# Performance work log

Hardware: AMD Instinct MI355X
Metric: run time of the kernel (lower is better)

The kernel has to match this reference:

```python
import jax, jax.numpy as jnp
import numpy as np

# Neighbor offsets (di, dj) implied by each 3x3 kernel: out_j = gray - shift(gray, di, dj)
# kernel0..kernel7 as defined in the torch module (center weight +1, one neighbor -1)
OFFSETS = [(0, -1), (1, -1), (1, 0), (1, 1), (0, 1), (-1, 1), (-1, 0), (-1, -1)]
EPS = 1e-5  # torch InstanceNorm2d default


def setup_inputs() -> dict:
    key = jax.random.key(0)
    x = jax.random.uniform(key, (8, 3, 1024, 1024), dtype=jnp.float32)
    return {"x": x}


def _ltpe(x):
    # RGB -> gray, [B,1,H,W]
    g = (0.3 * x[:, 0] + 0.59 * x[:, 1] + 0.11 * x[:, 2])[:, None]
    B, _, H, W = g.shape
    gp = jnp.pad(g, ((0, 0), (0, 0), (1, 1), (1, 1)))  # zero pad = conv padding=1
    out = jnp.zeros_like(g)
    for j, (di, dj) in enumerate(OFFSETS):
        nb = gp[:, :, 1 + di:1 + di + H, 1 + dj:1 + dj + W]
        d = (g - nb + 1.0) * 0.5          # (conv_out + 1) * 0.5
        out = out + d * (float(2 ** j) / 255.0)
    # InstanceNorm2d(1): per (b, c) mean/biased-var over spatial dims, no affine
    mean = jnp.mean(out, axis=(2, 3), keepdims=True)
    var = jnp.var(out, axis=(2, 3), keepdims=True)
    out = (out - mean) * jax.lax.rsqrt(var + EPS)
    return jnp.concatenate([out, out, out], axis=1)  # [B,3,H,W]


def reference(x):
    return _ltpe(x)
```

## Files before the change

kernel.cpp:

```cpp
#include <hip/hip_runtime.h>
#include <math.h>

constexpr int H = 1024, W = 1024, B = 8;
constexpr int NPIX = H * W;

__device__ __forceinline__ float grayat(const float* __restrict__ xb, int r, int c) {
    const float* p = xb + (size_t)r * W + c;
    return 0.3f * p[0] + 0.59f * p[NPIX] + 0.11f * p[2 * NPIX];
}

__global__ __launch_bounds__(256)
void ltpe_stage1(const float* __restrict__ x, float* __restrict__ out,
                 float2* __restrict__ part)
{
    const int b    = blockIdx.y;
    const int k    = blockIdx.x;
    const int r    = ((k & 7) << 7) | (k >> 3);
    const int tid  = threadIdx.x;
    const int c    = tid << 2;
    const int lane = tid & 63;

    const float* xb = x + (size_t)b * 3 * NPIX;

    float4 g[3];
    #pragma unroll
    for (int dr = 0; dr < 3; ++dr) {
        const int rr = r + dr - 1;
        float4 q0 = {0.f,0.f,0.f,0.f}, q1 = q0, q2 = q0;
        if ((unsigned)rr < (unsigned)H) {
            const float* p = xb + (size_t)rr * W + c;
            q0 = *reinterpret_cast<const float4*>(p);
            q1 = *reinterpret_cast<const float4*>(p + NPIX);
            q2 = *reinterpret_cast<const float4*>(p + 2 * NPIX);
        }
        g[dr].x = 0.3f * q0.x + 0.59f * q1.x + 0.11f * q2.x;
        g[dr].y = 0.3f * q0.y + 0.59f * q1.y + 0.11f * q2.y;
        g[dr].z = 0.3f * q0.z + 0.59f * q1.z + 0.11f * q2.z;
        g[dr].w = 0.3f * q0.w + 0.59f * q1.w + 0.11f * q2.w;
    }

    float gl[3], gr[3];
    #pragma unroll
    for (int dr = 0; dr < 3; ++dr) {
        gl[dr] = __shfl_up(g[dr].w, 1);
        gr[dr] = __shfl_down(g[dr].x, 1);
    }
    if (lane == 0) {
        #pragma unroll
        for (int dr = 0; dr < 3; ++dr) {
            const int rr = r + dr - 1;
            gl[dr] = (c > 0 && (unsigned)rr < (unsigned)H) ? grayat(xb, rr, c - 1) : 0.f;
        }
    }
    if (lane == 63) {
        #pragma unroll
        for (int dr = 0; dr < 3; ++dr) {
            const int rr = r + dr - 1;
            gr[dr] = (c + 4 < W && (unsigned)rr < (unsigned)H) ? grayat(xb, rr, c + 4) : 0.f;
        }
    }

    float up[6], mi[6], dn[6];
    up[0]=gl[0]; up[1]=g[0].x; up[2]=g[0].y; up[3]=g[0].z; up[4]=g[0].w; up[5]=gr[0];
    mi[0]=gl[1]; mi[1]=g[1].x; mi[2]=g[1].y; mi[3]=g[1].z; mi[4]=g[1].w; mi[5]=gr[1];
    dn[0]=gl[2]; dn[1]=g[2].x; dn[2]=g[2].y; dn[3]=g[2].z; dn[4]=g[2].w; dn[5]=gr[2];

    constexpr float w0 = 1.f/255.f,  w1 = 2.f/255.f,  w2 = 4.f/255.f,  w3 = 8.f/255.f,
                    w4 = 16.f/255.f, w5 = 32.f/255.f, w6 = 64.f/255.f, w7 = 128.f/255.f;
    float tv[4];
    #pragma unroll
    for (int kk = 0; kk < 4; ++kk) {
        float s = w0 * mi[kk];
        s = fmaf(w1, dn[kk],     s);
        s = fmaf(w2, dn[kk + 1], s);
        s = fmaf(w3, dn[kk + 2], s);
        s = fmaf(w4, mi[kk + 2], s);
        s = fmaf(w5, up[kk + 2], s);
        s = fmaf(w6, up[kk + 1], s);
        s = fmaf(w7, up[kk],     s);
        tv[kk] = 0.5f * mi[kk + 1] + 0.5f - 0.5f * s;
    }

    float4 t4 = {tv[0], tv[1], tv[2], tv[3]};
    *reinterpret_cast<float4*>(out + (size_t)b * 3 * NPIX + (size_t)r * W + c) = t4;

    float s  = tv[0] + tv[1] + tv[2] + tv[3];
    float ss = tv[0]*tv[0] + tv[1]*tv[1] + tv[2]*tv[2] + tv[3]*tv[3];
    #pragma unroll
    for (int off = 32; off >= 1; off >>= 1) {
        s  += __shfl_down(s, off);
        ss += __shfl_down(ss, off);
    }
    __shared__ float2 wred[4];
    if (lane == 0) wred[tid >> 6] = make_float2(s, ss);
    __syncthreads();
    if (tid == 0) {
        float2 a0 = wred[0], a1 = wred[1], a2 = wred[2], a3 = wred[3];
        part[(size_t)b * H + k] = make_float2(a0.x + a1.x + a2.x + a3.x,
                                              a0.y + a1.y + a2.y + a3.y);
    }
}

__global__ __launch_bounds__(256)
void ltpe_stage2(const float2* __restrict__ part, float* __restrict__ scal)
{
    const int b = blockIdx.x;
    const int tid = threadIdx.x;
    double s = 0.0, ss = 0.0;
    #pragma unroll
    for (int i = 0; i < 4; ++i) {
        float2 p = part[(size_t)b * H + tid + i * 256];
        s += (double)p.x; ss += (double)p.y;
    }
    #pragma unroll
    for (int off = 32; off >= 1; off >>= 1) {
        s  += __shfl_down(s, off);
        ss += __shfl_down(ss, off);
    }
    __shared__ double red[8];
    const int lane = tid & 63, wv = tid >> 6;
    if (lane == 0) { red[wv] = s; red[4 + wv] = ss; }
    __syncthreads();
    if (tid == 0) {
        const double S  = red[0] + red[1] + red[2] + red[3];
        const double SS = red[4] + red[5] + red[6] + red[7];
        const double n    = (double)NPIX;
        const double mean = S / n;
        const double var  = SS / n - mean * mean;
        scal[2 * b]     = (float)mean;
        scal[2 * b + 1] = (float)(1.0 / sqrt(var + 1e-5));
    }
}

__global__ __launch_bounds__(256)
void ltpe_stage3(float* __restrict__ out, const float* __restrict__ scal)
{
    const int b = blockIdx.y;
    const float mean = scal[2 * b];
    const float rstd = scal[2 * b + 1];
    const size_t base = (size_t)b * 3 * NPIX +
                        ((size_t)blockIdx.x * 256 + threadIdx.x) * 4;
    const float4 t4 = *reinterpret_cast<const float4*>(out + base);
    float4 y;
    y.x = (t4.x - mean) * rstd;
    y.y = (t4.y - mean) * rstd;
    y.z = (t4.z - mean) * rstd;
    y.w = (t4.w - mean) * rstd;
    *reinterpret_cast<float4*>(out + base)            = y;
    *reinterpret_cast<float4*>(out + base + NPIX)     = y;
    *reinterpret_cast<float4*>(out + base + 2 * NPIX) = y;
}

extern "C" void kernel_launch(void* const* d_in, const int* in_sizes, int n_in,
                              void* d_out, int out_size, void* d_ws, size_t ws_size,
                              hipStream_t stream)
{
    const float* x = (const float*)d_in[0];
    float* out = (float*)d_out;
    float2* part = (float2*)d_ws;
    float* scal  = (float*)((char*)d_ws + 65536);

    ltpe_stage1<<<dim3(H, B), 256, 0, stream>>>(x, out, part);
    ltpe_stage2<<<B, 256, 0, stream>>>(part, scal);
    ltpe_stage3<<<dim3(NPIX / 1024, B), 256, 0, stream>>>(out, scal);
}
```

Measured before the change: 55.93 us.

## Compute four rows per block in stage1 to reuse halo rows

Each stage1 block now handles four consecutive output rows and loads six input rows instead of three per row. This cuts redundant halo reads from 3x to 1.5x of the input and reduces the number of partial sums and blocks. The launch-bound occupancy hint is raised, and the stage2 reduction shrinks to one partial per thread. The trade-offs are higher register pressure from holding 18 float4 loads in flight and fewer total blocks (2048).

```diff
diff --git a/kernel.cpp b/kernel.cpp
--- a/kernel.cpp
+++ b/kernel.cpp
@@ -3,89 +3,99 @@
 
 constexpr int H = 1024, W = 1024, B = 8;
 constexpr int NPIX = H * W;
+constexpr int ROWS = 4;
+constexpr int RG   = H / ROWS;
 
 __device__ __forceinline__ float grayat(const float* __restrict__ xb, int r, int c) {
     const float* p = xb + (size_t)r * W + c;
     return 0.3f * p[0] + 0.59f * p[NPIX] + 0.11f * p[2 * NPIX];
 }
 
-__global__ __launch_bounds__(256)
+__global__ __launch_bounds__(256, 2)
 void ltpe_stage1(const float* __restrict__ x, float* __restrict__ out,
                  float2* __restrict__ part)
 {
     const int b    = blockIdx.y;
-    const int k    = blockIdx.x;
-    const int r    = ((k & 7) << 7) | (k >> 3);
+    const int r0   = blockIdx.x * ROWS;
     const int tid  = threadIdx.x;
     const int c    = tid << 2;
     const int lane = tid & 63;
-
     const float* xb = x + (size_t)b * 3 * NPIX;
 
-    float4 g[3];
+    float4 q[6][3];
     #pragma unroll
-    for (int dr = 0; dr < 3; ++dr) {
-        const int rr = r + dr - 1;
-        float4 q0 = {0.f,0.f,0.f,0.f}, q1 = q0, q2 = q0;
+    for (int i = 0; i < 6; ++i) {
+        const int rr = r0 - 1 + i;
+        float4 z = {0.f, 0.f, 0.f, 0.f};
+        q[i][0] = z; q[i][1] = z; q[i][2] = z;
         if ((unsigned)rr < (unsigned)H) {
             const float* p = xb + (size_t)rr * W + c;
-            q0 = *reinterpret_cast<const float4*>(p);
-            q1 = *reinterpret_cast<const float4*>(p + NPIX);
-            q2 = *reinterpret_cast<const float4*>(p + 2 * NPIX);
-        }
-        g[dr].x = 0.3f * q0.x + 0.59f * q1.x + 0.11f * q2.x;
-        g[dr].y = 0.3f * q0.y + 0.59f * q1.y + 0.11f * q2.y;
-        g[dr].z = 0.3f * q0.z + 0.59f * q1.z + 0.11f * q2.z;
-        g[dr].w = 0.3f * q0.w + 0.59f * q1.w + 0.11f * q2.w;
-    }
-
-    float gl[3], gr[3];
-    #pragma unroll
-    for (int dr = 0; dr < 3; ++dr) {
-        gl[dr] = __shfl_up(g[dr].w, 1);
-        gr[dr] = __shfl_down(g[dr].x, 1);
-    }
-    if (lane == 0) {
-        #pragma unroll
-        for (int dr = 0; dr < 3; ++dr) {
-            const int rr = r + dr - 1;
-            gl[dr] = (c > 0 && (unsigned)rr < (unsigned)H) ? grayat(xb, rr, c - 1) : 0.f;
+            q[i][0] = *reinterpret_cast<const float4*>(p);
+            q[i][1] = *reinterpret_cast<const float4*>(p + NPIX);
+            q[i][2] = *reinterpret_cast<const float4*>(p + 2 * NPIX);
         }
     }
-    if (lane == 63) {
+    float pl[6], pr[6];
+    #pragma unroll
+    for (int i = 0; i < 6; ++i) { pl[i] = 0.f; pr[i] = 0.f; }
+    if (lane == 0 && c > 0) {
         #pragma unroll
-        for (int dr = 0; dr < 3; ++dr) {
-            const int rr = r + dr - 1;
-            gr[dr] = (c + 4 < W && (unsigned)rr < (unsigned)H) ? grayat(xb, rr, c + 4) : 0.f;
+        for (int i = 0; i < 6; ++i) {
+            const int rr = r0 - 1 + i;
+            if ((unsigned)rr < (unsigned)H) pl[i] = grayat(xb, rr, c - 1);
+        }
+    }
+    if (lane == 63 && c + 4 < W) {
+        #pragma unroll
+        for (int i = 0; i < 6; ++i) {
+            const int rr = r0 - 1 + i;
+            if ((unsigned)rr < (unsigned)H) pr[i] = grayat(xb, rr, c + 4);
         }
     }
 
-    float up[6], mi[6], dn[6];
-    up[0]=gl[0]; up[1]=g[0].x; up[2]=g[0].y; up[3]=g[0].z; up[4]=g[0].w; up[5]=gr[0];
-    mi[0]=gl[1]; mi[1]=g[1].x; mi[2]=g[1].y; mi[3]=g[1].z; mi[4]=g[1].w; mi[5]=gr[1];
-    dn[0]=gl[2]; dn[1]=g[2].x; dn[2]=g[2].y; dn[3]=g[2].z; dn[4]=g[2].w; dn[5]=gr[2];
+    float g[6][6];
+    #pragma unroll
+    for (int i = 0; i < 6; ++i) {
+        const float4 a = q[i][0], d = q[i][1], e = q[i][2];
+        g[i][1] = 0.3f * a.x + 0.59f * d.x + 0.11f * e.x;
+        g[i][2] = 0.3f * a.y + 0.59f * d.y + 0.11f * e.y;
+        g[i][3] = 0.3f * a.z + 0.59f * d.z + 0.11f * e.z;
+        g[i][4] = 0.3f * a.w + 0.59f * d.w + 0.11f * e.w;
+        float l  = __shfl_up(g[i][4], 1);
+        float rt = __shfl_down(g[i][1], 1);
+        if (lane == 0)  l  = pl[i];
+        if (lane == 63) rt = pr[i];
+        g[i][0] = l; g[i][5] = rt;
+    }
 
     constexpr float w0 = 1.f/255.f,  w1 = 2.f/255.f,  w2 = 4.f/255.f,  w3 = 8.f/255.f,
                     w4 = 16.f/255.f, w5 = 32.f/255.f, w6 = 64.f/255.f, w7 = 128.f/255.f;
-    float tv[4];
+    float s = 0.f, ss = 0.f;
+    float* ob = out + (size_t)b * 3 * NPIX + (size_t)r0 * W + c;
     #pragma unroll
-    for (int kk = 0; kk < 4; ++kk) {
-        float s = w0 * mi[kk];
-        s = fmaf(w1, dn[kk],     s);
-        s = fmaf(w2, dn[kk + 1], s);
-        s = fmaf(w3, dn[kk + 2], s);
-        s = fmaf(w4, mi[kk + 2], s);
-        s = fmaf(w5, up[kk + 2], s);
-        s = fmaf(w6, up[kk + 1], s);
-        s = fmaf(w7, up[kk],     s);
-        tv[kk] = 0.5f * mi[kk + 1] + 0.5f - 0.5f * s;
+    for (int rr = 0; rr < ROWS; ++rr) {
+        const float (&up)[6] = g[rr];
+        const float (&mi)[6] = g[rr + 1];
+        const float (&dn)[6] = g[rr + 2];
+        float tv[4];
+        #pragma unroll
+        for (int kk = 0; kk < 4; ++kk) {
+            float sv = w0 * mi[kk];
+            sv = fmaf(w1, dn[kk],     sv);
+            sv = fmaf(w2, dn[kk + 1], sv);
+            sv = fmaf(w3, dn[kk + 2], sv);
+            sv = fmaf(w4, mi[kk + 2], sv);
+            sv = fmaf(w5, up[kk + 2], sv);
+            sv = fmaf(w6, up[kk + 1], sv);
+            sv = fmaf(w7, up[kk],     sv);
+            tv[kk] = 0.5f * mi[kk + 1] + 0.5f - 0.5f * sv;
+            s += tv[kk];
+            ss = fmaf(tv[kk], tv[kk], ss);
+        }
+        float4 t4 = {tv[0], tv[1], tv[2], tv[3]};
+        *reinterpret_cast<float4*>(ob + (size_t)rr * W) = t4;
     }
 
-    float4 t4 = {tv[0], tv[1], tv[2], tv[3]};
-    *reinterpret_cast<float4*>(out + (size_t)b * 3 * NPIX + (size_t)r * W + c) = t4;
-
-    float s  = tv[0] + tv[1] + tv[2] + tv[3];
-    float ss = tv[0]*tv[0] + tv[1]*tv[1] + tv[2]*tv[2] + tv[3]*tv[3];
     #pragma unroll
     for (int off = 32; off >= 1; off >>= 1) {
         s  += __shfl_down(s, off);
@@ -96,8 +106,8 @@
     __syncthreads();
     if (tid == 0) {
         float2 a0 = wred[0], a1 = wred[1], a2 = wred[2], a3 = wred[3];
-        part[(size_t)b * H + k] = make_float2(a0.x + a1.x + a2.x + a3.x,
-                                              a0.y + a1.y + a2.y + a3.y);
+        part[(size_t)b * RG + blockIdx.x] =
+            make_float2(a0.x + a1.x + a2.x + a3.x, a0.y + a1.y + a2.y + a3.y);
     }
 }
 
@@ -106,12 +116,8 @@
 {
     const int b = blockIdx.x;
     const int tid = threadIdx.x;
-    double s = 0.0, ss = 0.0;
-    #pragma unroll
-    for (int i = 0; i < 4; ++i) {
-        float2 p = part[(size_t)b * H + tid + i * 256];
-        s += (double)p.x; ss += (double)p.y;
-    }
+    const float2 p = part[(size_t)b * RG + tid];
+    double s = (double)p.x, ss = (double)p.y;
     #pragma unroll
     for (int off = 32; off >= 1; off >>= 1) {
         s  += __shfl_down(s, off);
@@ -158,9 +164,9 @@
     const float* x = (const float*)d_in[0];
     float* out = (float*)d_out;
     float2* part = (float2*)d_ws;
-    float* scal  = (float*)((char*)d_ws + 65536);
+    float* scal  = (float*)((char*)d_ws + 16384);
 
-    ltpe_stage1<<<dim3(H, B), 256, 0, stream>>>(x, out, part);
+    ltpe_stage1<<<dim3(RG, B), 256, 0, stream>>>(x, out, part);
     ltpe_stage2<<<B, 256, 0, stream>>>(part, scal);
     ltpe_stage3<<<dim3(NPIX / 1024, B), 256, 0, stream>>>(out, scal);
 }
```

Measured after the change: 63.28 us. 13.1% more time.
